# Kernel optimization log

Measured on AMD Instinct MI355X. Metric: run time of the kernel, lower is better.

## Reference

```python
import jax, jax.numpy as jnp
import numpy as np

B, N, NB, C, CZ = 4, 1024, 32, 384, 128
EPS = 1e-6


def setup_inputs() -> dict:
    key = jax.random.key(0)
    k1, k2, k3, k4, k5 = jax.random.split(key, 5)
    s_i = jax.random.normal(k1, (B, N, C), dtype=jnp.float32)
    s_ij = jax.random.normal(k2, (B, N, NB, C), dtype=jnp.float32)
    m_ij = jnp.ones((B, N, NB), dtype=jnp.float32)
    z_ij = jax.random.normal(k3, (B, N, NB, CZ), dtype=jnp.float32)
    W_s = jax.random.normal(k4, (C, C), dtype=jnp.float32) / np.sqrt(C)
    W_z = jax.random.normal(k5, (CZ, C), dtype=jnp.float32) / np.sqrt(CZ)
    gamma = jnp.ones((C,), dtype=jnp.float32)
    beta = jnp.zeros((C,), dtype=jnp.float32)
    return {"s_i": s_i, "s_ij": s_ij, "m_ij": m_ij, "z_ij": z_ij,
            "W_s": W_s, "W_z": W_z, "gamma": gamma, "beta": beta}


def reference(s_i, s_ij, m_ij, z_ij, W_s, W_z, gamma, beta):
    # Dense projection of neighbor single act: (B,N,n,C) @ (C,C)
    s_proj = jnp.einsum('bnkc,cd->bnkd', s_ij, W_s)
    # subtract center single act
    diff = s_proj - s_i[..., None, :]
    # gate by projected pair act: (B,N,n,Cz) @ (Cz,C)
    gate = jnp.einsum('bnkz,zd->bnkd', z_ij, W_z)
    msg = diff * gate
    # masked sum over neighbor axis
    s_new = jnp.sum(msg * m_ij[..., None], axis=-2)  # (B,N,C)
    # layernorm over last axis
    mu = jnp.mean(s_new, axis=-1, keepdims=True)
    var = jnp.mean(jnp.square(s_new - mu), axis=-1, keepdims=True)
    s_new = (s_new - mu) * jax.lax.rsqrt(var + EPS) * gamma + beta
    return s_new
```

## Files before the change

kernel.cpp:

```cpp
#include <hip/hip_runtime.h>
#include <hip/hip_bf16.h>

#define B_ 4
#define N_ 1024
#define NB_ 32
#define C_ 384
#define CZ_ 128
#define NSITES (B_ * N_)
#define EPSV 1e-6f
#define PAD 40

typedef unsigned short u16;
typedef unsigned int u32;
typedef __bf16 bf16x8 __attribute__((ext_vector_type(8)));
typedef float f32x4 __attribute__((ext_vector_type(4)));

__device__ __forceinline__ u16 f2bf(float f) {
    return __builtin_bit_cast(u16, __float2bfloat16(f));
}
__device__ __forceinline__ float bfbits2f(u16 u) {
    union { float f; u32 i; } x;
    x.i = ((u32)u) << 16;
    return x.f;
}

__global__ void prep_weights(const float* __restrict__ Ws, const float* __restrict__ Wz,
                             u16* __restrict__ Wts, u16* __restrict__ Wtz) {
    int idx = blockIdx.x * 256 + threadIdx.x;
    if (idx < C_ * C_) {
        int d = idx / C_, c = idx % C_;
        Wts[idx] = f2bf(Ws[c * C_ + d]);
    } else {
        int j = idx - C_ * C_;
        if (j < C_ * CZ_) {
            int d = j / CZ_, z = j % CZ_;
            Wtz[j] = f2bf(Wz[z * C_ + d]);
        }
    }
}

__global__ __launch_bounds__(256, 2)
void fused_msg_kernel(const float* __restrict__ s_i,
                      const float* __restrict__ s_ij,
                      const float* __restrict__ m_ij,
                      const float* __restrict__ z_ij,
                      const u16* __restrict__ Wts,
                      const u16* __restrict__ Wtz,
                      const float* __restrict__ gamma,
                      const float* __restrict__ beta,
                      float* __restrict__ out) {
    __shared__ u16 ldsW[C_ * PAD];
    __shared__ u16 ldsA[64 * PAD];
    __shared__ float lds_si[2 * C_];
    __shared__ float lds_m[64];
    __shared__ float lds_snew[2 * C_];

    const int tid = threadIdx.x;
    const int wave = tid >> 6;
    const int lane = tid & 63;
    const int q = lane >> 4;
    const int ln = lane & 15;
    const int colbase = wave * 96;

    const int site0 = blockIdx.x * 2;
    const long rowbase = (long)site0 * NB_;

    for (int i = tid; i < 2 * C_; i += 256)
        lds_si[i] = s_i[(long)site0 * C_ + i];
    if (tid < 64) lds_m[tid] = m_ij[rowbase + tid];

    const f32x4 ZERO = {0.f, 0.f, 0.f, 0.f};
    f32x4 acc[4][6];
    #pragma unroll
    for (int mt = 0; mt < 4; ++mt)
        #pragma unroll
        for (int nt = 0; nt < 6; ++nt)
            acc[mt][nt] = ZERO;

    #pragma unroll 1
    for (int kc = 0; kc < CZ_; kc += 32) {
        int s = tid;
        #pragma unroll
        for (int i = 0; i < 6; ++i) {
            int row = s >> 2, seg = s & 3;
            uint4 v = *reinterpret_cast<const uint4*>(Wtz + row * CZ_ + kc + seg * 8);
            *reinterpret_cast<uint4*>(&ldsW[row * PAD + seg * 8]) = v;
            s += 256;
        }
        {
            int row = tid >> 2, seg = tid & 3;
            const float* src = z_ij + (rowbase + row) * CZ_ + kc + seg * 8;
            float4 v0 = *reinterpret_cast<const float4*>(src);
            float4 v1 = *reinterpret_cast<const float4*>(src + 4);
            uint4 h;
            h.x = ((u32)f2bf(v0.y) << 16) | f2bf(v0.x);
            h.y = ((u32)f2bf(v0.w) << 16) | f2bf(v0.z);
            h.z = ((u32)f2bf(v1.y) << 16) | f2bf(v1.x);
            h.w = ((u32)f2bf(v1.w) << 16) | f2bf(v1.z);
            *reinterpret_cast<uint4*>(&ldsA[row * PAD + seg * 8]) = h;
        }
        __syncthreads();
        bf16x8 a[4];
        #pragma unroll
        for (int mt = 0; mt < 4; ++mt)
            a[mt] = *reinterpret_cast<const bf16x8*>(&ldsA[(mt * 16 + ln) * PAD + q * 8]);
        #pragma unroll
        for (int nt = 0; nt < 6; ++nt) {
            bf16x8 b = *reinterpret_cast<const bf16x8*>(&ldsW[(colbase + nt * 16 + ln) * PAD + q * 8]);
            #pragma unroll
            for (int mt = 0; mt < 4; ++mt)
                acc[mt][nt] = __builtin_amdgcn_mfma_f32_16x16x32_bf16(a[mt], b, acc[mt][nt], 0, 0, 0);
        }
        __syncthreads();
    }

    u32 gateb[4][6][2];
    #pragma unroll
    for (int mt = 0; mt < 4; ++mt) {
        float m0 = lds_m[mt * 16 + q * 4 + 0];
        float m1 = lds_m[mt * 16 + q * 4 + 1];
        float m2 = lds_m[mt * 16 + q * 4 + 2];
        float m3 = lds_m[mt * 16 + q * 4 + 3];
        #pragma unroll
        for (int nt = 0; nt < 6; ++nt) {
            gateb[mt][nt][0] = ((u32)f2bf(acc[mt][nt][1] * m1) << 16) | f2bf(acc[mt][nt][0] * m0);
            gateb[mt][nt][1] = ((u32)f2bf(acc[mt][nt][3] * m3) << 16) | f2bf(acc[mt][nt][2] * m2);
            acc[mt][nt] = ZERO;
        }
    }

    #pragma unroll 1
    for (int kc = 0; kc < C_; kc += 32) {
        int s = tid;
        #pragma unroll
        for (int i = 0; i < 6; ++i) {
            int row = s >> 2, seg = s & 3;
            uint4 v = *reinterpret_cast<const uint4*>(Wts + row * C_ + kc + seg * 8);
            *reinterpret_cast<uint4*>(&ldsW[row * PAD + seg * 8]) = v;
            s += 256;
        }
        {
            int row = tid >> 2, seg = tid & 3;
            const float* src = s_ij + (rowbase + row) * C_ + kc + seg * 8;
            float4 v0 = *reinterpret_cast<const float4*>(src);
            float4 v1 = *reinterpret_cast<const float4*>(src + 4);
            uint4 h;
            h.x = ((u32)f2bf(v0.y) << 16) | f2bf(v0.x);
            h.y = ((u32)f2bf(v0.w) << 16) | f2bf(v0.z);
            h.z = ((u32)f2bf(v1.y) << 16) | f2bf(v1.x);
            h.w = ((u32)f2bf(v1.w) << 16) | f2bf(v1.z);
            *reinterpret_cast<uint4*>(&ldsA[row * PAD + seg * 8]) = h;
        }
        __syncthreads();
        bf16x8 a[4];
        #pragma unroll
        for (int mt = 0; mt < 4; ++mt)
            a[mt] = *reinterpret_cast<const bf16x8*>(&ldsA[(mt * 16 + ln) * PAD + q * 8]);
        #pragma unroll
        for (int nt = 0; nt < 6; ++nt) {
            bf16x8 b = *reinterpret_cast<const bf16x8*>(&ldsW[(colbase + nt * 16 + ln) * PAD + q * 8]);
            #pragma unroll
            for (int mt = 0; mt < 4; ++mt)
                acc[mt][nt] = __builtin_amdgcn_mfma_f32_16x16x32_bf16(a[mt], b, acc[mt][nt], 0, 0, 0);
        }
        __syncthreads();
    }

    #pragma unroll
    for (int site = 0; site < 2; ++site) {
        #pragma unroll
        for (int nt = 0; nt < 6; ++nt) {
            int col = colbase + nt * 16 + ln;
            float si = lds_si[site * C_ + col];
            float p = 0.f;
            #pragma unroll
            for (int mh = 0; mh < 2; ++mh) {
                int mt = site * 2 + mh;
                #pragma unroll
                for (int r = 0; r < 4; ++r) {
                    float g = bfbits2f((u16)(gateb[mt][nt][r >> 1] >> ((r & 1) * 16)));
                    p += (acc[mt][nt][r] - si) * g;
                }
            }
            p += __shfl_xor(p, 16, 64);
            p += __shfl_xor(p, 32, 64);
            if (q == 0) lds_snew[site * C_ + col] = p;
        }
    }
    __syncthreads();

    if (wave < 2) {
        const int site = wave;
        float v[6];
        float sum = 0.f, sumsq = 0.f;
        #pragma unroll
        for (int i = 0; i < 6; ++i) {
            v[i] = lds_snew[site * C_ + lane + i * 64];
            sum += v[i];
            sumsq += v[i] * v[i];
        }
        #pragma unroll
        for (int off = 32; off >= 1; off >>= 1) {
            sum += __shfl_xor(sum, off, 64);
            sumsq += __shfl_xor(sumsq, off, 64);
        }
        float mu = sum * (1.f / C_);
        float var = sumsq * (1.f / C_) - mu * mu;
        float rs = rsqrtf(var + EPSV);
        #pragma unroll
        for (int i = 0; i < 6; ++i) {
            int col = lane + i * 64;
            out[(long)(site0 + site) * C_ + col] = (v[i] - mu) * rs * gamma[col] + beta[col];
        }
    }
}

extern "C" void kernel_launch(void* const* d_in, const int* in_sizes, int n_in,
                              void* d_out, int out_size, void* d_ws, size_t ws_size,
                              hipStream_t stream) {
    (void)in_sizes; (void)n_in; (void)out_size; (void)ws_size;
    const float* s_i   = (const float*)d_in[0];
    const float* s_ij  = (const float*)d_in[1];
    const float* m_ij  = (const float*)d_in[2];
    const float* z_ij  = (const float*)d_in[3];
    const float* W_s   = (const float*)d_in[4];
    const float* W_z   = (const float*)d_in[5];
    const float* gamma = (const float*)d_in[6];
    const float* beta  = (const float*)d_in[7];
    float* out = (float*)d_out;

    u16* wts = (u16*)d_ws;
    u16* wtz = wts + C_ * C_;

    int prep_elems = C_ * C_ + C_ * CZ_;
    prep_weights<<<(prep_elems + 255) / 256, 256, 0, stream>>>(W_s, W_z, wts, wtz);
    fused_msg_kernel<<<NSITES / 2, 256, 0, stream>>>(s_i, s_ij, m_ij, z_ij, wts, wtz,
                                                     gamma, beta, out);
}
```

Baseline: 439.5 us.

## Double-buffer global loads and process four sites per 512-thread block

Each block now handles four sites with 512 threads (two M-groups of waves sharing one weight tile). Global loads for the next K-chunk are issued into registers before the current chunk's MFMAs and committed to a double-buffered A tile in LDS afterwards. The intent is to hide global-load latency behind compute and to halve how many times each block reloads weight tiles per site. The cost is more registers per thread, more LDS, and an extra barrier per chunk, which may lower occupancy.

```diff
diff --git a/kernel.cpp b/kernel.cpp
--- a/kernel.cpp
+++ b/kernel.cpp
@@ -9,6 +9,9 @@
 #define NSITES (B_ * N_)
 #define EPSV 1e-6f
 #define PAD 40
+#define SPB 4
+#define MROWS 128
+#define THREADS 512
 
 typedef unsigned short u16;
 typedef unsigned int u32;
@@ -39,7 +42,59 @@
     }
 }
 
-__global__ __launch_bounds__(256, 2)
+struct Stage {
+    uint4 w0, w1, w2;
+    float4 a0, a1;
+};
+
+__device__ __forceinline__ void issue_stage(Stage& st, const u16* __restrict__ Wt, int kdim,
+                                            const float* __restrict__ A, long rowbase,
+                                            int kc, int tid) {
+    int ar = tid >> 2, ag = tid & 3;
+    const float* src = A + (rowbase + ar) * (long)kdim + kc + ag * 8;
+    st.a0 = *reinterpret_cast<const float4*>(src);
+    st.a1 = *reinterpret_cast<const float4*>(src + 4);
+    int s = tid;
+    st.w0 = *reinterpret_cast<const uint4*>(Wt + (s >> 2) * kdim + kc + (s & 3) * 8);
+    s = tid + 512;
+    st.w1 = *reinterpret_cast<const uint4*>(Wt + (s >> 2) * kdim + kc + (s & 3) * 8);
+    s = tid + 1024;
+    st.w2 = *reinterpret_cast<const uint4*>(Wt + (s >> 2) * kdim + kc + (s & 3) * 8);
+}
+
+__device__ __forceinline__ void commit_stage(const Stage& st, u16* ldsW, u16* ldsA, int tid) {
+    int s = tid;
+    *reinterpret_cast<uint4*>(&ldsW[(s >> 2) * PAD + (s & 3) * 8]) = st.w0;
+    s = tid + 512;
+    *reinterpret_cast<uint4*>(&ldsW[(s >> 2) * PAD + (s & 3) * 8]) = st.w1;
+    s = tid + 1024;
+    *reinterpret_cast<uint4*>(&ldsW[(s >> 2) * PAD + (s & 3) * 8]) = st.w2;
+    int ar = tid >> 2, ag = tid & 3;
+    uint4 h;
+    h.x = ((u32)f2bf(st.a0.y) << 16) | f2bf(st.a0.x);
+    h.y = ((u32)f2bf(st.a0.w) << 16) | f2bf(st.a0.z);
+    h.z = ((u32)f2bf(st.a1.y) << 16) | f2bf(st.a1.x);
+    h.w = ((u32)f2bf(st.a1.w) << 16) | f2bf(st.a1.z);
+    *reinterpret_cast<uint4*>(&ldsA[ar * PAD + ag * 8]) = h;
+}
+
+__device__ __forceinline__ void compute_chunk(const u16* ldsW, const u16* ldsA,
+                                              f32x4 (&acc)[4][6],
+                                              int mg, int colbase, int ln, int q) {
+    bf16x8 a[4];
+    #pragma unroll
+    for (int mt = 0; mt < 4; ++mt)
+        a[mt] = *reinterpret_cast<const bf16x8*>(&ldsA[(mg * 64 + mt * 16 + ln) * PAD + q * 8]);
+    #pragma unroll
+    for (int nt = 0; nt < 6; ++nt) {
+        bf16x8 b = *reinterpret_cast<const bf16x8*>(&ldsW[(colbase + nt * 16 + ln) * PAD + q * 8]);
+        #pragma unroll
+        for (int mt = 0; mt < 4; ++mt)
+            acc[mt][nt] = __builtin_amdgcn_mfma_f32_16x16x32_bf16(a[mt], b, acc[mt][nt], 0, 0, 0);
+    }
+}
+
+__global__ __launch_bounds__(THREADS, 2)
 void fused_msg_kernel(const float* __restrict__ s_i,
                       const float* __restrict__ s_ij,
                       const float* __restrict__ m_ij,
@@ -50,24 +105,25 @@
                       const float* __restrict__ beta,
                       float* __restrict__ out) {
     __shared__ u16 ldsW[C_ * PAD];
-    __shared__ u16 ldsA[64 * PAD];
-    __shared__ float lds_si[2 * C_];
-    __shared__ float lds_m[64];
-    __shared__ float lds_snew[2 * C_];
+    __shared__ u16 ldsA[2][MROWS * PAD];
+    __shared__ float lds_si[SPB * C_];
+    __shared__ float lds_m[MROWS];
+    __shared__ float lds_snew[SPB * C_];
 
     const int tid = threadIdx.x;
     const int wave = tid >> 6;
     const int lane = tid & 63;
     const int q = lane >> 4;
     const int ln = lane & 15;
-    const int colbase = wave * 96;
-
-    const int site0 = blockIdx.x * 2;
+    const int mg = wave >> 2;
+    const int colbase = (wave & 3) * 96;
+
+    const int site0 = blockIdx.x * SPB;
     const long rowbase = (long)site0 * NB_;
 
-    for (int i = tid; i < 2 * C_; i += 256)
+    for (int i = tid; i < SPB * C_; i += THREADS)
         lds_si[i] = s_i[(long)site0 * C_ + i];
-    if (tid < 64) lds_m[tid] = m_ij[rowbase + tid];
+    if (tid < MROWS) lds_m[tid] = m_ij[rowbase + tid];
 
     const f32x4 ZERO = {0.f, 0.f, 0.f, 0.f};
     f32x4 acc[4][6];
@@ -77,50 +133,33 @@
         for (int nt = 0; nt < 6; ++nt)
             acc[mt][nt] = ZERO;
 
-    #pragma unroll 1
-    for (int kc = 0; kc < CZ_; kc += 32) {
-        int s = tid;
-        #pragma unroll
-        for (int i = 0; i < 6; ++i) {
-            int row = s >> 2, seg = s & 3;
-            uint4 v = *reinterpret_cast<const uint4*>(Wtz + row * CZ_ + kc + seg * 8);
-            *reinterpret_cast<uint4*>(&ldsW[row * PAD + seg * 8]) = v;
-            s += 256;
-        }
-        {
-            int row = tid >> 2, seg = tid & 3;
-            const float* src = z_ij + (rowbase + row) * CZ_ + kc + seg * 8;
-            float4 v0 = *reinterpret_cast<const float4*>(src);
-            float4 v1 = *reinterpret_cast<const float4*>(src + 4);
-            uint4 h;
-            h.x = ((u32)f2bf(v0.y) << 16) | f2bf(v0.x);
-            h.y = ((u32)f2bf(v0.w) << 16) | f2bf(v0.z);
-            h.z = ((u32)f2bf(v1.y) << 16) | f2bf(v1.x);
-            h.w = ((u32)f2bf(v1.w) << 16) | f2bf(v1.z);
-            *reinterpret_cast<uint4*>(&ldsA[row * PAD + seg * 8]) = h;
-        }
+    Stage st;
+
+    {
+        const int NK = CZ_ / 32;
+        issue_stage(st, Wtz, CZ_, z_ij, rowbase, 0, tid);
+        commit_stage(st, ldsW, ldsA[0], tid);
         __syncthreads();
-        bf16x8 a[4];
-        #pragma unroll
-        for (int mt = 0; mt < 4; ++mt)
-            a[mt] = *reinterpret_cast<const bf16x8*>(&ldsA[(mt * 16 + ln) * PAD + q * 8]);
-        #pragma unroll
-        for (int nt = 0; nt < 6; ++nt) {
-            bf16x8 b = *reinterpret_cast<const bf16x8*>(&ldsW[(colbase + nt * 16 + ln) * PAD + q * 8]);
-            #pragma unroll
-            for (int mt = 0; mt < 4; ++mt)
-                acc[mt][nt] = __builtin_amdgcn_mfma_f32_16x16x32_bf16(a[mt], b, acc[mt][nt], 0, 0, 0);
-        }
-        __syncthreads();
+        #pragma unroll 2
+        for (int c = 0; c < NK; ++c) {
+            if (c + 1 < NK) issue_stage(st, Wtz, CZ_, z_ij, rowbase, (c + 1) * 32, tid);
+            compute_chunk(ldsW, ldsA[c & 1], acc, mg, colbase, ln, q);
+            __syncthreads();
+            if (c + 1 < NK) {
+                commit_stage(st, ldsW, ldsA[(c + 1) & 1], tid);
+                __syncthreads();
+            }
+        }
     }
 
     u32 gateb[4][6][2];
     #pragma unroll
     for (int mt = 0; mt < 4; ++mt) {
-        float m0 = lds_m[mt * 16 + q * 4 + 0];
-        float m1 = lds_m[mt * 16 + q * 4 + 1];
-        float m2 = lds_m[mt * 16 + q * 4 + 2];
-        float m3 = lds_m[mt * 16 + q * 4 + 3];
+        int rb = mg * 64 + mt * 16 + q * 4;
+        float m0 = lds_m[rb + 0];
+        float m1 = lds_m[rb + 1];
+        float m2 = lds_m[rb + 2];
+        float m3 = lds_m[rb + 3];
         #pragma unroll
         for (int nt = 0; nt < 6; ++nt) {
             gateb[mt][nt][0] = ((u32)f2bf(acc[mt][nt][1] * m1) << 16) | f2bf(acc[mt][nt][0] * m0);
@@ -129,45 +168,26 @@
         }
     }
 
-    #pragma unroll 1
-    for (int kc = 0; kc < C_; kc += 32) {
-        int s = tid;
-        #pragma unroll
-        for (int i = 0; i < 6; ++i) {
-            int row = s >> 2, seg = s & 3;
-            uint4 v = *reinterpret_cast<const uint4*>(Wts + row * C_ + kc + seg * 8);
-            *reinterpret_cast<uint4*>(&ldsW[row * PAD + seg * 8]) = v;
-            s += 256;
-        }
-        {
-            int row = tid >> 2, seg = tid & 3;
-            const float* src = s_ij + (rowbase + row) * C_ + kc + seg * 8;
-            float4 v0 = *reinterpret_cast<const float4*>(src);
-            float4 v1 = *reinterpret_cast<const float4*>(src + 4);
-            uint4 h;
-            h.x = ((u32)f2bf(v0.y) << 16) | f2bf(v0.x);
-            h.y = ((u32)f2bf(v0.w) << 16) | f2bf(v0.z);
-            h.z = ((u32)f2bf(v1.y) << 16) | f2bf(v1.x);
-            h.w = ((u32)f2bf(v1.w) << 16) | f2bf(v1.z);
-            *reinterpret_cast<uint4*>(&ldsA[row * PAD + seg * 8]) = h;
-        }
+    {
+        const int NK = C_ / 32;
+        issue_stage(st, Wts, C_, s_ij, rowbase, 0, tid);
+        commit_stage(st, ldsW, ldsA[0], tid);
         __syncthreads();
-        bf16x8 a[4];
-        #pragma unroll
-        for (int mt = 0; mt < 4; ++mt)
-            a[mt] = *reinterpret_cast<const bf16x8*>(&ldsA[(mt * 16 + ln) * PAD + q * 8]);
-        #pragma unroll
-        for (int nt = 0; nt < 6; ++nt) {
-            bf16x8 b = *reinterpret_cast<const bf16x8*>(&ldsW[(colbase + nt * 16 + ln) * PAD + q * 8]);
-            #pragma unroll
-            for (int mt = 0; mt < 4; ++mt)
-                acc[mt][nt] = __builtin_amdgcn_mfma_f32_16x16x32_bf16(a[mt], b, acc[mt][nt], 0, 0, 0);
-        }
-        __syncthreads();
-    }
-
-    #pragma unroll
-    for (int site = 0; site < 2; ++site) {
+        #pragma unroll 2
+        for (int c = 0; c < NK; ++c) {
+            if (c + 1 < NK) issue_stage(st, Wts, C_, s_ij, rowbase, (c + 1) * 32, tid);
+            compute_chunk(ldsW, ldsA[c & 1], acc, mg, colbase, ln, q);
+            __syncthreads();
+            if (c + 1 < NK) {
+                commit_stage(st, ldsW, ldsA[(c + 1) & 1], tid);
+                __syncthreads();
+            }
+        }
+    }
+
+    #pragma unroll
+    for (int sl = 0; sl < 2; ++sl) {
+        int site = mg * 2 + sl;
         #pragma unroll
         for (int nt = 0; nt < 6; ++nt) {
             int col = colbase + nt * 16 + ln;
@@ -175,7 +195,7 @@
             float p = 0.f;
             #pragma unroll
             for (int mh = 0; mh < 2; ++mh) {
-                int mt = site * 2 + mh;
+                int mt = sl * 2 + mh;
                 #pragma unroll
                 for (int r = 0; r < 4; ++r) {
                     float g = bfbits2f((u16)(gateb[mt][nt][r >> 1] >> ((r & 1) * 16)));
@@ -189,7 +209,7 @@
     }
     __syncthreads();
 
-    if (wave < 2) {
+    if (wave < SPB) {
         const int site = wave;
         float v[6];
         float sum = 0.f, sumsq = 0.f;
@@ -234,6 +254,6 @@
 
     int prep_elems = C_ * C_ + C_ * CZ_;
     prep_weights<<<(prep_elems + 255) / 256, 256, 0, stream>>>(W_s, W_z, wts, wtz);
-    fused_msg_kernel<<<NSITES / 2, 256, 0, stream>>>(s_i, s_ij, m_ij, z_ij, wts, wtz,
-                                                     gamma, beta, out);
-}
+    fused_msg_kernel<<<NSITES / SPB, THREADS, 0, stream>>>(s_i, s_ij, m_ij, z_ij, wts, wtz,
+                                                           gamma, beta, out);
+}
```

Result: no change. 447.3 us (+1.8%).
